# Kernel tuning notes

Measured on AMD Instinct MI355X. Metric: run time of the kernel, lower is better.

Reference implementation:

```python
import jax, jax.numpy as jnp
import numpy as np

N, E = 50000, 800000
NFEAT, HID, NHEAD, NCLASS = 256, 32, 8, 40
NEG_SLOPE = 0.2


def gat_conv(x, src, dst, W, a_src, a_dst, bias, heads, out_ch, concat):
    n = x.shape[0]
    h = (x @ W).reshape(n, heads, out_ch)              # [N, H, C]
    alpha_src = jnp.einsum('nhc,hc->nh', h, a_src)     # [N, H]
    alpha_dst = jnp.einsum('nhc,hc->nh', h, a_dst)
    e = jax.nn.leaky_relu(alpha_src[src] + alpha_dst[dst], NEG_SLOPE)  # [E, H]
    # segment softmax over incoming edges of each dst node
    m = jax.ops.segment_max(e, dst, num_segments=n)
    ex = jnp.exp(e - m[dst])
    s = jax.ops.segment_sum(ex, dst, num_segments=n)
    alpha = ex / (s[dst] + 1e-16)                      # [E, H]
    out = jax.ops.segment_sum(h[src] * alpha[:, :, None], dst, num_segments=n)  # [N, H, C]
    out = out.reshape(n, heads * out_ch) if concat else out.mean(axis=1)
    return out + bias


def setup_inputs() -> dict:
    key = jax.random.key(0)
    ks = jax.random.split(key, 12)
    x = jax.random.normal(ks[0], (N, NFEAT), dtype=jnp.float32)
    edge_index = jax.random.randint(ks[1], (2, E), 0, N, dtype=jnp.int64)
    edge_attr = jax.random.normal(ks[2], (E, 8), dtype=jnp.float32)  # unused by the model
    s1 = 1.0 / np.sqrt(NFEAT)
    s2 = 1.0 / np.sqrt(HID * NHEAD)
    W1 = jax.random.normal(ks[3], (NFEAT, NHEAD * HID), dtype=jnp.float32) * s1
    att_src1 = jax.random.normal(ks[4], (NHEAD, HID), dtype=jnp.float32) * 0.1
    att_dst1 = jax.random.normal(ks[5], (NHEAD, HID), dtype=jnp.float32) * 0.1
    b1 = jnp.zeros((NHEAD * HID,), dtype=jnp.float32)
    W2 = jax.random.normal(ks[6], (NHEAD * HID, NCLASS), dtype=jnp.float32) * s2
    att_src2 = jax.random.normal(ks[7], (1, NCLASS), dtype=jnp.float32) * 0.1
    att_dst2 = jax.random.normal(ks[8], (1, NCLASS), dtype=jnp.float32) * 0.1
    b2 = jnp.zeros((NCLASS,), dtype=jnp.float32)
    return {"x": x, "edge_index": edge_index, "edge_attr": edge_attr,
            "W1": W1, "att_src1": att_src1, "att_dst1": att_dst1, "b1": b1,
            "W2": W2, "att_src2": att_src2, "att_dst2": att_dst2, "b2": b2}


def reference(x, edge_index, edge_attr, W1, att_src1, att_dst1, b1, W2, att_src2, att_dst2, b2):
    # eval mode: dropout is identity. GATConv adds self-loops by default.
    n = x.shape[0]
    loops = jnp.arange(n, dtype=edge_index.dtype)
    src = jnp.concatenate([edge_index[0], loops])
    dst = jnp.concatenate([edge_index[1], loops])
    h = jax.nn.elu(gat_conv(x, src, dst, W1, att_src1, att_dst1, b1, NHEAD, HID, True))
    final = gat_conv(h, src, dst, W2, att_src2, att_dst2, b2, 1, NCLASS, False)
    return final, jax.nn.log_softmax(final, axis=1)
```

## Files before the change

### kernel.cpp

```cpp
#include <hip/hip_runtime.h>
#include <hip/hip_bf16.h>
#include <math.h>

#define NN 50000
#define EE 800000
#define ET 850000
#define F1 256
#define NHEAD 8
#define HID 32
#define NCLASS 40
#define NEG 0.2f

typedef __attribute__((ext_vector_type(8))) short short8_t;
typedef __attribute__((ext_vector_type(4))) float float4_t;

__device__ __forceinline__ int clampN(int v) {
    return v < 0 ? 0 : (v >= NN ? NN - 1 : v);
}
__device__ __forceinline__ unsigned short f2bf(float f) {
    __hip_bfloat16 h = __float2bfloat16(f);
    return __builtin_bit_cast(unsigned short, h);
}
__device__ __forceinline__ float bf2f(unsigned short u) {
    return __uint_as_float((unsigned)u << 16);
}

__global__ __launch_bounds__(256) void hist_kernel(const int* __restrict__ ei, int* __restrict__ deg) {
    int t = blockIdx.x * 256 + threadIdx.x;
    if (t >= ET) return;
    int d = (t < EE) ? ei[EE + t] : (t - EE);
    d = clampN(d);
    atomicAdd(&deg[d], 1);
}

__global__ __launch_bounds__(256) void scan1_kernel(const int* __restrict__ deg, int* __restrict__ off, int* __restrict__ bsum) {
    __shared__ int lds[256];
    int b = blockIdx.x, tid = threadIdx.x;
    int base = b * 1024 + tid * 4;
    int v0 = (base + 0 < NN) ? deg[base + 0] : 0;
    int v1 = (base + 1 < NN) ? deg[base + 1] : 0;
    int v2 = (base + 2 < NN) ? deg[base + 2] : 0;
    int v3 = (base + 3 < NN) ? deg[base + 3] : 0;
    int s1 = v0 + v1, s2 = s1 + v2, s3 = s2 + v3;
    lds[tid] = s3;
    __syncthreads();
    for (int o = 1; o < 256; o <<= 1) {
        int t = (tid >= o) ? lds[tid - o] : 0;
        __syncthreads();
        if (tid >= o) lds[tid] += t;
        __syncthreads();
    }
    int excl = tid ? lds[tid - 1] : 0;
    if (base + 0 < NN) off[base + 1] = excl + v0;
    if (base + 1 < NN) off[base + 2] = excl + s1;
    if (base + 2 < NN) off[base + 3] = excl + s2;
    if (base + 3 < NN) off[base + 4] = excl + s3;
    if (tid == 255) bsum[b] = lds[255];
}

__global__ __launch_bounds__(256) void scan2_kernel(int* __restrict__ bsum, int nb) {
    __shared__ int lds[256];
    int tid = threadIdx.x;
    lds[tid] = (tid < nb) ? bsum[tid] : 0;
    __syncthreads();
    for (int o = 1; o < 256; o <<= 1) {
        int t = (tid >= o) ? lds[tid - o] : 0;
        __syncthreads();
        if (tid >= o) lds[tid] += t;
        __syncthreads();
    }
    if (tid < nb) bsum[tid] = lds[tid];
}

__global__ __launch_bounds__(256) void scan3_kernel(int* __restrict__ off, const int* __restrict__ bsum) {
    int b = blockIdx.x, tid = threadIdx.x;
    if (b == 0 && tid == 0) off[0] = 0;
    if (b == 0) return;
    int add = bsum[b - 1];
    int base = b * 1024 + tid * 4;
    #pragma unroll
    for (int i = 0; i < 4; ++i) {
        if (base + i < NN) off[base + i + 1] += add;
    }
}

__global__ __launch_bounds__(256) void scatter_kernel(const int* __restrict__ ei, const int* __restrict__ off,
                                                      int* __restrict__ cursor, int* __restrict__ esrc) {
    int t = blockIdx.x * 256 + threadIdx.x;
    if (t >= ET) return;
    int s, d;
    if (t < EE) { s = ei[t]; d = ei[EE + t]; }
    else        { s = t - EE; d = t - EE; }
    s = clampN(s); d = clampN(d);
    int p = off[d] + atomicAdd(&cursor[d], 1);
    esrc[p] = s;
}

__global__ __launch_bounds__(256) void prep_kernel(const float* __restrict__ W1,
                                                   const float* __restrict__ as1, const float* __restrict__ ad1,
                                                   unsigned short* __restrict__ Bh, unsigned short* __restrict__ Bl) {
    int n = blockIdx.x;
    int k = threadIdx.x;
    float v;
    if (n < 256) {
        v = W1[(size_t)k * 256 + n];
    } else {
        int j = n - 256;
        int h = j & 7;
        const float* att = (j < 8) ? (as1 + h * 32) : (ad1 + h * 32);
        float s = 0.f;
        #pragma unroll
        for (int c = 0; c < 32; ++c) s += W1[(size_t)k * 256 + h * 32 + c] * att[c];
        v = s;
    }
    unsigned short hi = f2bf(v);
    Bh[n * 256 + k] = hi;
    Bl[n * 256 + k] = f2bf(v - bf2f(hi));
}

#define AKP 40
__global__ __launch_bounds__(256, 2) void gemm1_kernel(const float* __restrict__ x,
                                                       const unsigned short* __restrict__ Bh,
                                                       const unsigned short* __restrict__ Bl,
                                                       unsigned short* __restrict__ h1b,
                                                       float* __restrict__ asrc1, float* __restrict__ adst1) {
    __shared__ __align__(16) unsigned short Ah[128 * AKP];
    __shared__ __align__(16) unsigned short Al[128 * AKP];
    __shared__ __align__(16) unsigned short Bhs[272 * AKP];
    __shared__ __align__(16) unsigned short Bls[272 * AKP];
    int tid = threadIdx.x;
    int wave = tid >> 6, lane = tid & 63;
    int quad = lane >> 4, l16 = lane & 15;
    int row0 = blockIdx.x * 128;

    float4_t acc[2][17];
    #pragma unroll
    for (int i = 0; i < 2; ++i)
        #pragma unroll
        for (int j = 0; j < 17; ++j) acc[i][j] = (float4_t){0.f, 0.f, 0.f, 0.f};

    for (int k0 = 0; k0 < 256; k0 += 32) {
        __syncthreads();
        #pragma unroll
        for (int i = 0; i < 4; ++i) {
            int id = i * 256 + tid;
            int r = id >> 3, kq = id & 7;
            int rr = row0 + r; if (rr >= NN) rr = NN - 1;
            float4 v = *(const float4*)(x + (size_t)rr * 256 + k0 + kq * 4);
            ushort4 hi, lo;
            hi.x = f2bf(v.x); lo.x = f2bf(v.x - bf2f(hi.x));
            hi.y = f2bf(v.y); lo.y = f2bf(v.y - bf2f(hi.y));
            hi.z = f2bf(v.z); lo.z = f2bf(v.z - bf2f(hi.z));
            hi.w = f2bf(v.w); lo.w = f2bf(v.w - bf2f(hi.w));
            *(ushort4*)(Ah + r * AKP + kq * 4) = hi;
            *(ushort4*)(Al + r * AKP + kq * 4) = lo;
        }
        for (int id = tid; id < 272 * 4; id += 256) {
            int r = id >> 2, kq = id & 3;
            *(float4*)(Bhs + r * AKP + kq * 8) = *(const float4*)(Bh + (size_t)r * 256 + k0 + kq * 8);
            *(float4*)(Bls + r * AKP + kq * 8) = *(const float4*)(Bl + (size_t)r * 256 + k0 + kq * 8);
        }
        __syncthreads();
        short8_t ah[2], al[2];
        #pragma unroll
        for (int mt = 0; mt < 2; ++mt) {
            int mrow = wave * 32 + mt * 16 + l16;
            ah[mt] = *(const short8_t*)(Ah + mrow * AKP + quad * 8);
            al[mt] = *(const short8_t*)(Al + mrow * AKP + quad * 8);
        }
        #pragma unroll
        for (int nt = 0; nt < 17; ++nt) {
            int nrow = nt * 16 + l16;
            short8_t bh  = *(const short8_t*)(Bhs + nrow * AKP + quad * 8);
            short8_t blo = *(const short8_t*)(Bls + nrow * AKP + quad * 8);
            #pragma unroll
            for (int mt = 0; mt < 2; ++mt) {
                acc[mt][nt] = __builtin_amdgcn_mfma_f32_16x16x32_bf16(ah[mt], bh,  acc[mt][nt], 0, 0, 0);
                acc[mt][nt] = __builtin_amdgcn_mfma_f32_16x16x32_bf16(ah[mt], blo, acc[mt][nt], 0, 0, 0);
                acc[mt][nt] = __builtin_amdgcn_mfma_f32_16x16x32_bf16(al[mt], bh,  acc[mt][nt], 0, 0, 0);
            }
        }
    }
    #pragma unroll
    for (int mt = 0; mt < 2; ++mt) {
        int rbase = row0 + wave * 32 + mt * 16 + quad * 4;
        #pragma unroll
        for (int r = 0; r < 4; ++r) {
            int row = rbase + r;
            if (row >= NN) continue;
            #pragma unroll
            for (int nt = 0; nt < 16; ++nt)
                h1b[(size_t)row * 256 + nt * 16 + l16] = f2bf(acc[mt][nt][r]);
            float v = acc[mt][16][r];
            if (l16 < 8) asrc1[row * 8 + l16] = v;
            else         adst1[row * 8 + (l16 - 8)] = v;
        }
    }
}

#define WST 68
__global__ __launch_bounds__(256) void agg1_kernel(const unsigned short* __restrict__ h1b, const float* __restrict__ asrc,
                                                   const float* __restrict__ adst, const int* __restrict__ esrc,
                                                   const int* __restrict__ off,
                                                   const float* __restrict__ b1, unsigned short* __restrict__ hout) {
    __shared__ __align__(16) float wl[4][8 * WST];
    __shared__ __align__(16) int  snl[4][64];
    int tid = threadIdx.x;
    int wave = tid >> 6;
    int wid = blockIdx.x * 4 + wave;
    if (wid >= NN) return;
    int lane = tid & 63;
    int hp = lane & 7;
    int jp = lane >> 3;
    int hc = lane >> 3;
    int c0 = lane * 4;
    float adh_p = adst[wid * 8 + hp];
    int e0 = off[wid], e1 = off[wid + 1];
    float* wlw = wl[wave];
    int* snw = snl[wave];
    const char* hb = (const char*)h1b;
    unsigned lofs = (unsigned)c0 * 2;

    float m = -INFINITY, s = 0.f;
    float ax = 0.f, ay = 0.f, az = 0.f, aw = 0.f;

    for (int base = e0; base < e1; base += 64) {
        int cnt = e1 - base; if (cnt > 64) cnt = 64;
        int snv = esrc[base + (lane < cnt ? lane : cnt - 1)];
        snw[lane] = snv;
        int nch = (cnt + 7) >> 3;
        float ee[8];
        float wmax = -INFINITY;
        #pragma unroll
        for (int cj = 0; cj < 8; ++cj) {
            if (cj >= nch) { ee[cj] = -INFINITY; continue; }
            int jedge = cj * 8 + jp;
            int sj = __shfl(snv, jedge);
            float a = asrc[sj * 8 + hp];
            float e = a + adh_p;
            e = (e >= 0.f) ? e : NEG * e;
            if (jedge >= cnt) e = -INFINITY;
            ee[cj] = e;
            wmax = fmaxf(wmax, e);
        }
        wmax = fmaxf(wmax, __shfl_xor(wmax, 8));
        wmax = fmaxf(wmax, __shfl_xor(wmax, 16));
        wmax = fmaxf(wmax, __shfl_xor(wmax, 32));
        float mn = fmaxf(m, wmax);
        float t = __expf(m - mn);
        m = mn;
        s *= t;
        float tc = __shfl(t, hc);
        ax *= tc; ay *= tc; az *= tc; aw *= tc;
        #pragma unroll
        for (int cj = 0; cj < 8; ++cj) {
            if (cj >= nch) break;
            float w = __expf(ee[cj] - mn);
            s += w;
            wlw[hp * WST + cj * 8 + jp] = w;
        }
        const float* wrow = wlw + hc * WST;
        for (int j = 0; j < cnt; j += 4) {
            float4 w4 = *(const float4*)(wrow + j);
            int4 sn4 = *(const int4*)(snw + j);
            uint2 u0 = *(const uint2*)(hb + (((unsigned)sn4.x << 9) + lofs));
            uint2 u1 = *(const uint2*)(hb + (((unsigned)sn4.y << 9) + lofs));
            uint2 u2 = *(const uint2*)(hb + (((unsigned)sn4.z << 9) + lofs));
            uint2 u3 = *(const uint2*)(hb + (((unsigned)sn4.w << 9) + lofs));
            ax += w4.x * __uint_as_float(u0.x << 16);
            ay += w4.x * __uint_as_float(u0.x & 0xFFFF0000u);
            az += w4.x * __uint_as_float(u0.y << 16);
            aw += w4.x * __uint_as_float(u0.y & 0xFFFF0000u);
            ax += w4.y * __uint_as_float(u1.x << 16);
            ay += w4.y * __uint_as_float(u1.x & 0xFFFF0000u);
            az += w4.y * __uint_as_float(u1.y << 16);
            aw += w4.y * __uint_as_float(u1.y & 0xFFFF0000u);
            ax += w4.z * __uint_as_float(u2.x << 16);
            ay += w4.z * __uint_as_float(u2.x & 0xFFFF0000u);
            az += w4.z * __uint_as_float(u2.y << 16);
            aw += w4.z * __uint_as_float(u2.y & 0xFFFF0000u);
            ax += w4.w * __uint_as_float(u3.x << 16);
            ay += w4.w * __uint_as_float(u3.x & 0xFFFF0000u);
            az += w4.w * __uint_as_float(u3.y << 16);
            aw += w4.w * __uint_as_float(u3.y & 0xFFFF0000u);
        }
    }
    s += __shfl_xor(s, 8);
    s += __shfl_xor(s, 16);
    s += __shfl_xor(s, 32);
    float sh = __shfl(s, hc);
    float inv = 1.f / (sh + 1e-16f);
    float4 b = *(const float4*)(b1 + c0);
    float vx = ax * inv + b.x, vy = ay * inv + b.y, vz = az * inv + b.z, vw = aw * inv + b.w;
    ushort4 o;
    o.x = f2bf((vx > 0.f) ? vx : expm1f(vx));
    o.y = f2bf((vy > 0.f) ? vy : expm1f(vy));
    o.z = f2bf((vz > 0.f) ? vz : expm1f(vz));
    o.w = f2bf((vw > 0.f) ? vw : expm1f(vw));
    *(ushort4*)(hout + (size_t)wid * 256 + c0) = o;
}

#define G2_TM 128
#define G2_KC 32
__global__ __launch_bounds__(256) void gemm2_kernel(const unsigned short* __restrict__ h, const float* __restrict__ W2,
                                                    const float* __restrict__ at_s, const float* __restrict__ at_d,
                                                    unsigned short* __restrict__ h2b, float* __restrict__ as2,
                                                    float* __restrict__ ad2) {
    __shared__ __align__(16) float w2s[256 * 40];
    __shared__ __align__(16) float As[G2_KC][132];
    int tid = threadIdx.x;
    for (int i = tid; i < 256 * 40; i += 256) w2s[i] = W2[i];
    int g  = tid & 7;
    int rg = tid >> 3;
    int row0 = blockIdx.x * G2_TM;
    float acc[4][5] = {};
    float ats[5], atd[5];
    #pragma unroll
    for (int j = 0; j < 5; ++j) { ats[j] = at_s[g + 8 * j]; atd[j] = at_d[g + 8 * j]; }

    for (int k0 = 0; k0 < 256; k0 += G2_KC) {
        __syncthreads();
        #pragma unroll
        for (int i = 0; i < 2; ++i) {
            int id = i * 256 + tid;
            int r  = id >> 2;
            int kq = id & 3;
            int rr = row0 + r; if (rr >= NN) rr = NN - 1;
            uint4 u = *(const uint4*)(h + (size_t)rr * 256 + k0 + kq * 8);
            As[kq * 8 + 0][r] = __uint_as_float(u.x << 16);
            As[kq * 8 + 1][r] = __uint_as_float(u.x & 0xFFFF0000u);
            As[kq * 8 + 2][r] = __uint_as_float(u.y << 16);
            As[kq * 8 + 3][r] = __uint_as_float(u.y & 0xFFFF0000u);
            As[kq * 8 + 4][r] = __uint_as_float(u.z << 16);
            As[kq * 8 + 5][r] = __uint_as_float(u.z & 0xFFFF0000u);
            As[kq * 8 + 6][r] = __uint_as_float(u.w << 16);
            As[kq * 8 + 7][r] = __uint_as_float(u.w & 0xFFFF0000u);
        }
        __syncthreads();
        #pragma unroll 4
        for (int k = 0; k < G2_KC; ++k) {
            float4 a = *(const float4*)(&As[k][rg * 4]);
            float w[5];
            #pragma unroll
            for (int j = 0; j < 5; ++j) w[j] = w2s[(k0 + k) * 40 + g + 8 * j];
            float av[4] = {a.x, a.y, a.z, a.w};
            #pragma unroll
            for (int r = 0; r < 4; ++r)
                #pragma unroll
                for (int j = 0; j < 5; ++j)
                    acc[r][j] += av[r] * w[j];
        }
    }

    #pragma unroll
    for (int r = 0; r < 4; ++r) {
        int row = row0 + rg * 4 + r;
        float ps = 0.f, pd = 0.f;
        #pragma unroll
        for (int j = 0; j < 5; ++j) {
            ps += acc[r][j] * ats[j];
            pd += acc[r][j] * atd[j];
        }
        ps += __shfl_xor(ps, 1); pd += __shfl_xor(pd, 1);
        ps += __shfl_xor(ps, 2); pd += __shfl_xor(pd, 2);
        ps += __shfl_xor(ps, 4); pd += __shfl_xor(pd, 4);
        if (row < NN) {
            #pragma unroll
            for (int j = 0; j < 5; ++j) h2b[(size_t)row * 40 + g + 8 * j] = f2bf(acc[r][j]);
            if (g == 0) { as2[row] = ps; ad2[row] = pd; }
        }
    }
}

__global__ __launch_bounds__(256) void agg2_kernel(const unsigned short* __restrict__ h2b, const float* __restrict__ asrc,
                                                   const float* __restrict__ adst, const int* __restrict__ esrc,
                                                   const int* __restrict__ off,
                                                   const float* __restrict__ b2, float* __restrict__ outF,
                                                   float* __restrict__ outL) {
    __shared__ __align__(16) float wl2[4][64];
    __shared__ __align__(16) int  snl2[4][64];
    int tid = threadIdx.x;
    int wave = tid >> 6;
    int wid = blockIdx.x * 4 + wave;
    if (wid >= NN) return;
    int lane = tid & 63;
    int c = lane;
    float adh = adst[wid];
    int e0 = off[wid], e1 = off[wid + 1];
    const char* hb = (const char*)h2b + ((unsigned)(c < NCLASS ? c : 0) << 1);
    float* wlw = wl2[wave];
    int* snw = snl2[wave];

    float m = -INFINITY, s = 0.f, acc = 0.f;

    for (int base = e0; base < e1; base += 64) {
        int cnt = e1 - base; if (cnt > 64) cnt = 64;
        int snv = esrc[base + (lane < cnt ? lane : cnt - 1)];
        snw[lane] = snv;
        float a = asrc[snv];
        float e = a + adh;
        e = (e >= 0.f) ? e : NEG * e;
        if (lane >= cnt) e = -INFINITY;
        float cm = e;
        cm = fmaxf(cm, __shfl_xor(cm, 1));
        cm = fmaxf(cm, __shfl_xor(cm, 2));
        cm = fmaxf(cm, __shfl_xor(cm, 4));
        cm = fmaxf(cm, __shfl_xor(cm, 8));
        cm = fmaxf(cm, __shfl_xor(cm, 16));
        cm = fmaxf(cm, __shfl_xor(cm, 32));
        float mn = fmaxf(m, cm);
        float t = __expf(m - mn);
        float w = __expf(e - mn);
        s = s * t + w;
        m = mn;
        wlw[lane] = w;
        acc *= t;
        for (int j = 0; j < cnt; j += 4) {
            float4 w4 = *(const float4*)(wlw + j);
            int4 sn4 = *(const int4*)(snw + j);
            unsigned short v0 = *(const unsigned short*)(hb + (unsigned)sn4.x * 80);
            unsigned short v1 = *(const unsigned short*)(hb + (unsigned)sn4.y * 80);
            unsigned short v2 = *(const unsigned short*)(hb + (unsigned)sn4.z * 80);
            unsigned short v3 = *(const unsigned short*)(hb + (unsigned)sn4.w * 80);
            acc += w4.x * bf2f(v0);
            acc += w4.y * bf2f(v1);
            acc += w4.z * bf2f(v2);
            acc += w4.w * bf2f(v3);
        }
    }
    s += __shfl_xor(s, 1);
    s += __shfl_xor(s, 2);
    s += __shfl_xor(s, 4);
    s += __shfl_xor(s, 8);
    s += __shfl_xor(s, 16);
    s += __shfl_xor(s, 32);
    float inv = 1.f / (s + 1e-16f);
    float fin = (c < NCLASS) ? (acc * inv + b2[c]) : -INFINITY;
    if (c < NCLASS) outF[(size_t)wid * 40 + c] = fin;
    float mx = fin;
    for (int o = 32; o; o >>= 1) mx = fmaxf(mx, __shfl_xor(mx, o));
    float ex = (c < NCLASS) ? __expf(fin - mx) : 0.f;
    float sm = ex;
    for (int o = 32; o; o >>= 1) sm += __shfl_xor(sm, o);
    if (c < NCLASS) outL[(size_t)wid * 40 + c] = fin - mx - __logf(sm);
}

extern "C" void kernel_launch(void* const* d_in, const int* in_sizes, int n_in,
                              void* d_out, int out_size, void* d_ws, size_t ws_size,
                              hipStream_t stream) {
    const float* x   = (const float*)d_in[0];
    const int*   ei  = (const int*)d_in[1];
    const float* W1  = (const float*)d_in[3];
    const float* as1 = (const float*)d_in[4];
    const float* ad1 = (const float*)d_in[5];
    const float* b1  = (const float*)d_in[6];
    const float* W2  = (const float*)d_in[7];
    const float* as2c = (const float*)d_in[8];
    const float* ad2c = (const float*)d_in[9];
    const float* b2  = (const float*)d_in[10];

    float* outF = (float*)d_out;
    float* outL = outF + (size_t)NN * NCLASS;

    char* w = (char*)d_ws;
    auto alloc = [&](size_t bytes) {
        void* p = (void*)w;
        w += (bytes + 255) & ~(size_t)255;
        return p;
    };
    unsigned short* h1b = (unsigned short*)alloc((size_t)NN * 256 * 2);
    unsigned short* hbuf = (unsigned short*)alloc((size_t)NN * 256 * 2);
    unsigned short* h2b = (unsigned short*)alloc((size_t)NN * 40 * 2);
    float* asrc1 = (float*)alloc((size_t)NN * 8 * 4);
    float* adst1 = (float*)alloc((size_t)NN * 8 * 4);
    float* asrc2 = (float*)alloc((size_t)NN * 4);
    float* adst2 = (float*)alloc((size_t)NN * 4);
    int* deg    = (int*)alloc((size_t)NN * 4);
    int* off    = (int*)alloc((size_t)(NN + 1) * 4);
    int* cursor = (int*)alloc((size_t)NN * 4);
    int* esrc   = (int*)alloc((size_t)ET * 4);
    int* bsum   = (int*)alloc(64 * 4);
    unsigned short* W1th = (unsigned short*)alloc((size_t)272 * 256 * 2);
    unsigned short* W1tl = (unsigned short*)alloc((size_t)272 * 256 * 2);

    const int NB_SCAN = (NN + 1023) / 1024;

    hipMemsetAsync(deg, 0, (size_t)NN * 4, stream);
    hipMemsetAsync(cursor, 0, (size_t)NN * 4, stream);

    hist_kernel<<<(ET + 255) / 256, 256, 0, stream>>>(ei, deg);
    scan1_kernel<<<NB_SCAN, 256, 0, stream>>>(deg, off, bsum);
    scan2_kernel<<<1, 256, 0, stream>>>(bsum, NB_SCAN);
    scan3_kernel<<<NB_SCAN, 256, 0, stream>>>(off, bsum);
    scatter_kernel<<<(ET + 255) / 256, 256, 0, stream>>>(ei, off, cursor, esrc);

    prep_kernel<<<272, 256, 0, stream>>>(W1, as1, ad1, W1th, W1tl);
    gemm1_kernel<<<(NN + 127) / 128, 256, 0, stream>>>(x, W1th, W1tl, h1b, asrc1, adst1);
    agg1_kernel<<<(NN + 3) / 4, 256, 0, stream>>>(h1b, asrc1, adst1, esrc, off, b1, hbuf);
    gemm2_kernel<<<(NN + G2_TM - 1) / G2_TM, 256, 0, stream>>>(hbuf, W2, as2c, ad2c, h2b, asrc2, adst2);
    agg2_kernel<<<(NN + 3) / 4, 256, 0, stream>>>(h2b, asrc2, adst2, esrc, off, b2, outF, outL);
}
```

Measured before the change: 373.9 us.

## Store intermediates as fp16 and reuse histogram atomic ranks in CSR scatter

```diff
diff --git a/kernel.cpp b/kernel.cpp
--- a/kernel.cpp
+++ b/kernel.cpp
@@ -1,5 +1,6 @@
 #include <hip/hip_runtime.h>
 #include <hip/hip_bf16.h>
+#include <hip/hip_fp16.h>
 #include <math.h>
 
 #define NN 50000
@@ -24,13 +25,29 @@
 __device__ __forceinline__ float bf2f(unsigned short u) {
     return __uint_as_float((unsigned)u << 16);
 }
-
-__global__ __launch_bounds__(256) void hist_kernel(const int* __restrict__ ei, int* __restrict__ deg) {
+__device__ __forceinline__ unsigned short f2h(float f) {
+    __half h = __float2half(f);
+    return __builtin_bit_cast(unsigned short, h);
+}
+__device__ __forceinline__ float h2f(unsigned short u) {
+    __half h = __builtin_bit_cast(__half, u);
+    return __half2float(h);
+}
+__device__ __forceinline__ float hlo2f(unsigned int u) {
+    return h2f((unsigned short)(u & 0xFFFFu));
+}
+__device__ __forceinline__ float hhi2f(unsigned int u) {
+    return h2f((unsigned short)(u >> 16));
+}
+
+__global__ __launch_bounds__(256) void hist_kernel(const int* __restrict__ ei, int* __restrict__ deg,
+                                                   unsigned int* __restrict__ pack) {
     int t = blockIdx.x * 256 + threadIdx.x;
     if (t >= ET) return;
     int d = (t < EE) ? ei[EE + t] : (t - EE);
     d = clampN(d);
-    atomicAdd(&deg[d], 1);
+    int r = atomicAdd(&deg[d], 1);
+    pack[t] = ((unsigned)d << 15) | (unsigned)r;
 }
 
 __global__ __launch_bounds__(256) void scan1_kernel(const int* __restrict__ deg, int* __restrict__ off, int* __restrict__ bsum) {
@@ -85,15 +102,15 @@
 }
 
 __global__ __launch_bounds__(256) void scatter_kernel(const int* __restrict__ ei, const int* __restrict__ off,
-                                                      int* __restrict__ cursor, int* __restrict__ esrc) {
+                                                      const unsigned int* __restrict__ pack, int* __restrict__ esrc) {
     int t = blockIdx.x * 256 + threadIdx.x;
     if (t >= ET) return;
-    int s, d;
-    if (t < EE) { s = ei[t]; d = ei[EE + t]; }
-    else        { s = t - EE; d = t - EE; }
-    s = clampN(s); d = clampN(d);
-    int p = off[d] + atomicAdd(&cursor[d], 1);
-    esrc[p] = s;
+    unsigned p = pack[t];
+    int d = p >> 15;
+    int r = p & 0x7FFF;
+    int s = (t < EE) ? ei[t] : (t - EE);
+    s = clampN(s);
+    esrc[off[d] + r] = s;
 }
 
 __global__ __launch_bounds__(256) void prep_kernel(const float* __restrict__ W1,
@@ -190,7 +207,7 @@
             if (row >= NN) continue;
             #pragma unroll
             for (int nt = 0; nt < 16; ++nt)
-                h1b[(size_t)row * 256 + nt * 16 + l16] = f2bf(acc[mt][nt][r]);
+                h1b[(size_t)row * 256 + nt * 16 + l16] = f2h(acc[mt][nt][r]);
             float v = acc[mt][16][r];
             if (l16 < 8) asrc1[row * 8 + l16] = v;
             else         adst1[row * 8 + (l16 - 8)] = v;
@@ -267,22 +284,22 @@
             uint2 u1 = *(const uint2*)(hb + (((unsigned)sn4.y << 9) + lofs));
             uint2 u2 = *(const uint2*)(hb + (((unsigned)sn4.z << 9) + lofs));
             uint2 u3 = *(const uint2*)(hb + (((unsigned)sn4.w << 9) + lofs));
-            ax += w4.x * __uint_as_float(u0.x << 16);
-            ay += w4.x * __uint_as_float(u0.x & 0xFFFF0000u);
-            az += w4.x * __uint_as_float(u0.y << 16);
-            aw += w4.x * __uint_as_float(u0.y & 0xFFFF0000u);
-            ax += w4.y * __uint_as_float(u1.x << 16);
-            ay += w4.y * __uint_as_float(u1.x & 0xFFFF0000u);
-            az += w4.y * __uint_as_float(u1.y << 16);
-            aw += w4.y * __uint_as_float(u1.y & 0xFFFF0000u);
-            ax += w4.z * __uint_as_float(u2.x << 16);
-            ay += w4.z * __uint_as_float(u2.x & 0xFFFF0000u);
-            az += w4.z * __uint_as_float(u2.y << 16);
-            aw += w4.z * __uint_as_float(u2.y & 0xFFFF0000u);
-            ax += w4.w * __uint_as_float(u3.x << 16);
-            ay += w4.w * __uint_as_float(u3.x & 0xFFFF0000u);
-            az += w4.w * __uint_as_float(u3.y << 16);
-            aw += w4.w * __uint_as_float(u3.y & 0xFFFF0000u);
+            ax += w4.x * hlo2f(u0.x);
+            ay += w4.x * hhi2f(u0.x);
+            az += w4.x * hlo2f(u0.y);
+            aw += w4.x * hhi2f(u0.y);
+            ax += w4.y * hlo2f(u1.x);
+            ay += w4.y * hhi2f(u1.x);
+            az += w4.y * hlo2f(u1.y);
+            aw += w4.y * hhi2f(u1.y);
+            ax += w4.z * hlo2f(u2.x);
+            ay += w4.z * hhi2f(u2.x);
+            az += w4.z * hlo2f(u2.y);
+            aw += w4.z * hhi2f(u2.y);
+            ax += w4.w * hlo2f(u3.x);
+            ay += w4.w * hhi2f(u3.x);
+            az += w4.w * hlo2f(u3.y);
+            aw += w4.w * hhi2f(u3.y);
         }
     }
     s += __shfl_xor(s, 8);
@@ -293,10 +310,10 @@
     float4 b = *(const float4*)(b1 + c0);
     float vx = ax * inv + b.x, vy = ay * inv + b.y, vz = az * inv + b.z, vw = aw * inv + b.w;
     ushort4 o;
-    o.x = f2bf((vx > 0.f) ? vx : expm1f(vx));
-    o.y = f2bf((vy > 0.f) ? vy : expm1f(vy));
-    o.z = f2bf((vz > 0.f) ? vz : expm1f(vz));
-    o.w = f2bf((vw > 0.f) ? vw : expm1f(vw));
+    o.x = f2h((vx > 0.f) ? vx : expm1f(vx));
+    o.y = f2h((vy > 0.f) ? vy : expm1f(vy));
+    o.z = f2h((vz > 0.f) ? vz : expm1f(vz));
+    o.w = f2h((vw > 0.f) ? vw : expm1f(vw));
     *(ushort4*)(hout + (size_t)wid * 256 + c0) = o;
 }
 
@@ -327,14 +344,14 @@
             int kq = id & 3;
             int rr = row0 + r; if (rr >= NN) rr = NN - 1;
             uint4 u = *(const uint4*)(h + (size_t)rr * 256 + k0 + kq * 8);
-            As[kq * 8 + 0][r] = __uint_as_float(u.x << 16);
-            As[kq * 8 + 1][r] = __uint_as_float(u.x & 0xFFFF0000u);
-            As[kq * 8 + 2][r] = __uint_as_float(u.y << 16);
-            As[kq * 8 + 3][r] = __uint_as_float(u.y & 0xFFFF0000u);
-            As[kq * 8 + 4][r] = __uint_as_float(u.z << 16);
-            As[kq * 8 + 5][r] = __uint_as_float(u.z & 0xFFFF0000u);
-            As[kq * 8 + 6][r] = __uint_as_float(u.w << 16);
-            As[kq * 8 + 7][r] = __uint_as_float(u.w & 0xFFFF0000u);
+            As[kq * 8 + 0][r] = hlo2f(u.x);
+            As[kq * 8 + 1][r] = hhi2f(u.x);
+            As[kq * 8 + 2][r] = hlo2f(u.y);
+            As[kq * 8 + 3][r] = hhi2f(u.y);
+            As[kq * 8 + 4][r] = hlo2f(u.z);
+            As[kq * 8 + 5][r] = hhi2f(u.z);
+            As[kq * 8 + 6][r] = hlo2f(u.w);
+            As[kq * 8 + 7][r] = hhi2f(u.w);
         }
         __syncthreads();
         #pragma unroll 4
@@ -366,7 +383,7 @@
         ps += __shfl_xor(ps, 4); pd += __shfl_xor(pd, 4);
         if (row < NN) {
             #pragma unroll
-            for (int j = 0; j < 5; ++j) h2b[(size_t)row * 40 + g + 8 * j] = f2bf(acc[r][j]);
+            for (int j = 0; j < 5; ++j) h2b[(size_t)row * 40 + g + 8 * j] = f2h(acc[r][j]);
             if (g == 0) { as2[row] = ps; ad2[row] = pd; }
         }
     }
@@ -422,10 +439,10 @@
             unsigned short v1 = *(const unsigned short*)(hb + (unsigned)sn4.y * 80);
             unsigned short v2 = *(const unsigned short*)(hb + (unsigned)sn4.z * 80);
             unsigned short v3 = *(const unsigned short*)(hb + (unsigned)sn4.w * 80);
-            acc += w4.x * bf2f(v0);
-            acc += w4.y * bf2f(v1);
-            acc += w4.z * bf2f(v2);
-            acc += w4.w * bf2f(v3);
+            acc += w4.x * h2f(v0);
+            acc += w4.y * h2f(v1);
+            acc += w4.z * h2f(v2);
+            acc += w4.w * h2f(v3);
         }
     }
     s += __shfl_xor(s, 1);
@@ -477,7 +494,7 @@
     float* adst2 = (float*)alloc((size_t)NN * 4);
     int* deg    = (int*)alloc((size_t)NN * 4);
     int* off    = (int*)alloc((size_t)(NN + 1) * 4);
-    int* cursor = (int*)alloc((size_t)NN * 4);
+    unsigned int* pack = (unsigned int*)alloc((size_t)ET * 4);
     int* esrc   = (int*)alloc((size_t)ET * 4);
     int* bsum   = (int*)alloc(64 * 4);
     unsigned short* W1th = (unsigned short*)alloc((size_t)272 * 256 * 2);
@@ -486,13 +503,12 @@
     const int NB_SCAN = (NN + 1023) / 1024;
 
     hipMemsetAsync(deg, 0, (size_t)NN * 4, stream);
-    hipMemsetAsync(cursor, 0, (size_t)NN * 4, stream);
-
-    hist_kernel<<<(ET + 255) / 256, 256, 0, stream>>>(ei, deg);
+
+    hist_kernel<<<(ET + 255) / 256, 256, 0, stream>>>(ei, deg, pack);
     scan1_kernel<<<NB_SCAN, 256, 0, stream>>>(deg, off, bsum);
     scan2_kernel<<<1, 256, 0, stream>>>(bsum, NB_SCAN);
     scan3_kernel<<<NB_SCAN, 256, 0, stream>>>(off, bsum);
-    scatter_kernel<<<(ET + 255) / 256, 256, 0, stream>>>(ei, off, cursor, esrc);
+    scatter_kernel<<<(ET + 255) / 256, 256, 0, stream>>>(ei, off, pack, esrc);
 
     prep_kernel<<<272, 256, 0, stream>>>(W1, as1, ad1, W1th, W1tl);
     gemm1_kernel<<<(NN + 127) / 128, 256, 0, stream>>>(x, W1th, W1tl, h1b, asrc1, adst1);
```

New measurement: 339.1 us. 9.3% less time.
